# Kernel tuning notes

Hardware: AMD Instinct MI355X
Metric: run time of the kernel (lower is better)

Reference implementation:

```python
import jax, jax.numpy as jnp
import numpy as np

B, S, I, H, O, L = 64, 2048, 256, 256, 256, 2


def setup_inputs() -> dict:
    key = jax.random.key(0)
    ks = jax.random.split(key, 9)
    return {
        "x": jax.random.normal(ks[0], (B, S, I), dtype=jnp.float32),
        "w_h0": jax.random.normal(ks[1], (I, H), dtype=jnp.float32) * 0.05,
        "u_h0": jax.random.normal(ks[2], (H, H), dtype=jnp.float32) * 0.05,
        "b_h0": jax.random.uniform(ks[3], (H,), dtype=jnp.float32),
        "w_h1": jax.random.normal(ks[4], (H, H), dtype=jnp.float32) * 0.05,
        "u_h1": jax.random.normal(ks[5], (H, H), dtype=jnp.float32) * 0.05,
        "b_h1": jax.random.uniform(ks[6], (H,), dtype=jnp.float32),
        "w_q": jax.random.normal(ks[7], (H, O), dtype=jnp.float32) * 0.05,
        "b_q": jnp.zeros((O,), dtype=jnp.float32),
    }


def reference(x, w_h0, u_h0, b_h0, w_h1, u_h1, b_h1, w_q, b_q):
    batch = x.shape[0]
    h0_init = jnp.zeros((batch, H), dtype=x.dtype)
    h1_init = jnp.zeros((batch, H), dtype=x.dtype)

    def step(carry, x_t):
        h0, h1 = carry  # each [B, H]
        h0n = jnp.tanh(x_t @ w_h0 + h0 @ u_h0 + b_h0)
        h1n = jnp.tanh(h0n @ w_h1 + h1 @ u_h1 + b_h1)
        y = h1n @ w_q + b_q  # [B, O]
        return (h0n, h1n), y

    (h0_f, h1_f), ys = jax.lax.scan(step, (h0_init, h1_init),
                                    jnp.swapaxes(x, 0, 1))  # xs: [S, B, I]
    out = jnp.swapaxes(ys, 0, 1)  # [B, S, O]
    h_final = jnp.stack([h0_f, h1_f], axis=1)  # [B, L, H]
    return out, h_final
```

## Files before the change

### kernel.cpp

```cpp
#include <hip/hip_runtime.h>

#define S_LEN 2048
#define NB    64
#define HD    256

typedef _Float16 half2_t  __attribute__((ext_vector_type(2)));
typedef _Float16 half8_t  __attribute__((ext_vector_type(8)));
typedef float    floatx4  __attribute__((ext_vector_type(4)));
typedef float    floatx8  __attribute__((ext_vector_type(8)));
typedef float    floatx16 __attribute__((ext_vector_type(16)));

__device__ __forceinline__ float fdot2(half2_t a, half2_t b, float c){
#if __has_builtin(__builtin_amdgcn_fdot2)
  return __builtin_amdgcn_fdot2(a, b, c, false);
#else
  return c + (float)a[0]*(float)b[0] + (float)a[1]*(float)b[1];
#endif
}

__device__ __forceinline__ float tanh_fast(float x){
  float e = __expf(2.0f * x);
  return 1.0f - 2.0f / (e + 1.0f);
}

#define MATVEC(HS, WREG, ACC)                                                     \
  {                                                                               \
    float a0_=0.f, a1_=0.f, a2_=0.f, a3_=0.f;                                     \
    _Pragma("unroll")                                                             \
    for (int i_ = 0; i_ < 32; ++i_){                                              \
      half8_t c_ = (HS)[i_];                                                      \
      a0_ = fdot2(__builtin_shufflevector(c_, c_, 0, 1), (WREG)[4*i_+0], a0_);    \
      a1_ = fdot2(__builtin_shufflevector(c_, c_, 2, 3), (WREG)[4*i_+1], a1_);    \
      a2_ = fdot2(__builtin_shufflevector(c_, c_, 4, 5), (WREG)[4*i_+2], a2_);    \
      a3_ = fdot2(__builtin_shufflevector(c_, c_, 6, 7), (WREG)[4*i_+3], a3_);    \
    }                                                                             \
    ACC = (a0_ + a1_) + (a2_ + a3_);                                              \
  }

__launch_bounds__(768)
__global__ void rnn_kernel(const _Float16* __restrict__ A0,
                           const float* __restrict__ u_h0,
                           const float* __restrict__ w_h1,
                           const float* __restrict__ u_h1,
                           const float* __restrict__ b_h1,
                           _Float16* __restrict__ H1,
                           float* __restrict__ hfinal)
{
  const int b    = blockIdx.x;
  const int tid  = threadIdx.x;
  const int wave = tid >> 6;
  const int lane = tid & 63;
  const int group = wave >> 2;
  const int col   = ((wave & 3) << 6) | lane;

  __shared__ __align__(16) _Float16 h0buf[2][HD];
  __shared__ __align__(16) _Float16 h1buf[2][HD];
  __shared__ __align__(16) float    wpart[2][HD];

  if (tid < HD){
    h0buf[0][tid] = (_Float16)0.f; h0buf[1][tid] = (_Float16)0.f;
    h1buf[0][tid] = (_Float16)0.f; h1buf[1][tid] = (_Float16)0.f;
    wpart[0][tid] = 0.f;           wpart[1][tid] = 0.f;
  }

  const float* Wm = (group == 0) ? u_h0 : (group == 1) ? u_h1 : w_h1;
  half2_t w[128];
  #pragma unroll
  for (int i = 0; i < 128; ++i){
    float w0 = Wm[(2*i)     * HD + col];
    float w1 = Wm[(2*i + 1) * HD + col];
    half2_t p; p[0] = (_Float16)w0; p[1] = (_Float16)w1;
    w[i] = p;
  }

  const size_t base = (size_t)b * S_LEN * HD;
  const float bias = (group == 1) ? b_h1[col] : 0.f;

  _Float16 a0p0 = (_Float16)0.f, a0p1 = (_Float16)0.f;
  if (group == 0){
    a0p0 = A0[base + 0 * HD + col];
    a0p1 = A0[base + 1 * HD + col];
  }

  __syncthreads();

  for (int tau = 0; tau < S_LEN + 2; ++tau){
    if (group == 0){
      if (tau < S_LEN){
        const half8_t* hs = (const half8_t*)(&h0buf[(tau + 1) & 1][0]);
        float acc; MATVEC(hs, w, acc);
        float h = tanh_fast(acc + (float)a0p0);
        h0buf[tau & 1][col] = (_Float16)h;
        if (tau == S_LEN - 1) hfinal[(b << 9) + col] = h;
        a0p0 = a0p1;
        if (tau + 2 < S_LEN) a0p1 = A0[base + (size_t)(tau + 2) * HD + col];
      }
    } else if (group == 2){
      const int t1 = tau - 1;
      if (t1 >= 0 && t1 < S_LEN){
        const half8_t* hs = (const half8_t*)(&h0buf[t1 & 1][0]);
        float acc; MATVEC(hs, w, acc);
        wpart[t1 & 1][col] = acc;
      }
    } else {
      const int t = tau - 2;
      if (t >= 0){
        const half8_t* hs = (const half8_t*)(&h1buf[(t + 1) & 1][0]);
        float acc; MATVEC(hs, w, acc);
        float h = tanh_fast(acc + wpart[t & 1][col] + bias);
        h1buf[t & 1][col] = (_Float16)h;
        H1[base + (size_t)t * HD + col] = (_Float16)h;
        if (t == S_LEN - 1) hfinal[(b << 9) + HD + col] = h;
      }
    }
    __syncthreads();
  }
}

__global__ void prep_kernel(const float* __restrict__ w0, const float* __restrict__ wq,
                            _Float16* __restrict__ B0, _Float16* __restrict__ Bq)
{
  int i = blockIdx.x * 256 + threadIdx.x;
  for (int idx = i; idx < 65536; idx += 64 * 256){
    int k = idx >> 8, n = idx & 255;
    int sw = (k >> 3) * 2048 + n * 8 + (k & 7);
    B0[sw] = (_Float16)w0[idx];
    Bq[sw] = (_Float16)wq[idx];
  }
}

template<bool A_FP32, bool C_FP16>
__launch_bounds__(512)
__global__ void gemm256(const void* __restrict__ Ap,
                        const _Float16* __restrict__ Bsw,
                        const float* __restrict__ bias,
                        void* __restrict__ Cp)
{
  const int wave = threadIdx.x >> 6;
  const int lane = threadIdx.x & 63;
  const int r  = lane & 31;
  const int hf = lane >> 5;
  const size_t rowt = (size_t)blockIdx.x * 256 + (size_t)wave * 32;

  floatx16 acc[8];
  #pragma unroll
  for (int i = 0; i < 8; ++i)
    #pragma unroll
    for (int j = 0; j < 16; ++j) acc[i][j] = 0.f;

  const size_t arow = rowt + (size_t)r;
  #pragma unroll
  for (int ks = 0; ks < 16; ++ks){
    half8_t af;
    if (A_FP32){
      const float* A = (const float*)Ap;
      const floatx4* p = (const floatx4*)(A + arow * 256 + ks * 16 + hf * 8);
      floatx4 v0 = p[0], v1 = p[1];
      floatx8 v = __builtin_shufflevector(v0, v1, 0, 1, 2, 3, 4, 5, 6, 7);
      af = __builtin_convertvector(v, half8_t);
    } else {
      const _Float16* A = (const _Float16*)Ap;
      af = *(const half8_t*)(A + arow * 256 + ks * 16 + hf * 8);
    }
    #pragma unroll
    for (int ct = 0; ct < 8; ++ct){
      half8_t bf = *(const half8_t*)(Bsw + (size_t)(ks * 2 + hf) * 2048 + (ct * 32 + r) * 8);
      acc[ct] = __builtin_amdgcn_mfma_f32_32x32x16_f16(af, bf, acc[ct], 0, 0, 0);
    }
  }

  #pragma unroll
  for (int ct = 0; ct < 8; ++ct){
    const int col = ct * 32 + r;
    const float bc = bias[col];
    #pragma unroll
    for (int reg = 0; reg < 16; ++reg){
      const int rl = (reg & 3) + 8 * (reg >> 2) + 4 * hf;
      const size_t idx = (rowt + rl) * 256 + col;
      float v = acc[ct][reg] + bc;
      if (C_FP16) ((_Float16*)Cp)[idx] = (_Float16)v;
      else        ((float*)Cp)[idx]    = v;
    }
  }
}

extern "C" void kernel_launch(void* const* d_in, const int* in_sizes, int n_in,
                              void* d_out, int out_size, void* d_ws, size_t ws_size,
                              hipStream_t stream)
{
  (void)in_sizes; (void)n_in; (void)out_size;

  const float* x    = (const float*)d_in[0];
  const float* w_h0 = (const float*)d_in[1];
  const float* u_h0 = (const float*)d_in[2];
  const float* b_h0 = (const float*)d_in[3];
  const float* w_h1 = (const float*)d_in[4];
  const float* u_h1 = (const float*)d_in[5];
  const float* b_h1 = (const float*)d_in[6];
  const float* w_q  = (const float*)d_in[7];
  const float* b_q  = (const float*)d_in[8];

  const size_t MSH = (size_t)NB * S_LEN * HD;
  float* y    = (float*)d_out;
  float* hfin = y + MSH;

  _Float16* H1 = (_Float16*)d_ws;
  _Float16 *A0, *B0sw, *Bqsw;
  if (ws_size >= (MSH * 2 + 2 * 65536) * sizeof(_Float16)){
    A0   = H1 + MSH;
    B0sw = A0 + MSH;
    Bqsw = B0sw + 65536;
  } else {
    A0   = (_Float16*)d_out;
    B0sw = H1 + MSH;
    Bqsw = B0sw + 65536;
  }

  prep_kernel<<<dim3(64), dim3(256), 0, stream>>>(w_h0, w_q, B0sw, Bqsw);
  gemm256<true, true><<<dim3(512), dim3(512), 0, stream>>>((const void*)x, B0sw, b_h0, (void*)A0);
  rnn_kernel<<<dim3(NB), dim3(768), 0, stream>>>(A0, u_h0, w_h1, u_h1, b_h1, H1, hfin);
  gemm256<false, false><<<dim3(512), dim3(512), 0, stream>>>((const void*)H1, Bqsw, b_q, (void*)y);
}
```

Before: 2.665 ms.

## Split RNN layers into separate pipelined blocks synchronized via global flags

Replaces the single per-batch block, which ran all three matvec stages per timestep behind a block barrier, with three blocks per batch, one per stage. The blocks communicate through global ring buffers and acquire/release progress counters. This lets the layer-0 recurrence, the layer-1 input projection and the layer-1 recurrence run concurrently on different CUs. In exchange, each step adds cross-CU global-memory handoff latency and spin-waiting, and correctness depends on all blocks being co-resident.

```diff
diff --git a/kernel.cpp b/kernel.cpp
--- a/kernel.cpp
+++ b/kernel.cpp
@@ -1,8 +1,11 @@
 #include <hip/hip_runtime.h>
+#include <stdint.h>
 
 #define S_LEN 2048
 #define NB    64
 #define HD    256
+#define RING  1024
+#define RMASK 1023
 
 typedef _Float16 half2_t  __attribute__((ext_vector_type(2)));
 typedef _Float16 half8_t  __attribute__((ext_vector_type(8)));
@@ -37,33 +40,31 @@
     ACC = (a0_ + a1_) + (a2_ + a3_);                                              \
   }
 
-__launch_bounds__(768)
-__global__ void rnn_kernel(const _Float16* __restrict__ A0,
-                           const float* __restrict__ u_h0,
-                           const float* __restrict__ w_h1,
-                           const float* __restrict__ u_h1,
-                           const float* __restrict__ b_h1,
-                           _Float16* __restrict__ H1,
-                           float* __restrict__ hfinal)
-{
-  const int b    = blockIdx.x;
-  const int tid  = threadIdx.x;
-  const int wave = tid >> 6;
-  const int lane = tid & 63;
-  const int group = wave >> 2;
-  const int col   = ((wave & 3) << 6) | lane;
-
-  __shared__ __align__(16) _Float16 h0buf[2][HD];
-  __shared__ __align__(16) _Float16 h1buf[2][HD];
-  __shared__ __align__(16) float    wpart[2][HD];
-
-  if (tid < HD){
-    h0buf[0][tid] = (_Float16)0.f; h0buf[1][tid] = (_Float16)0.f;
-    h1buf[0][tid] = (_Float16)0.f; h1buf[1][tid] = (_Float16)0.f;
-    wpart[0][tid] = 0.f;           wpart[1][tid] = 0.f;
-  }
-
-  const float* Wm = (group == 0) ? u_h0 : (group == 1) ? u_h1 : w_h1;
+__launch_bounds__(256, 1)
+__global__ void rnn_pipe(const _Float16* __restrict__ A0,
+                         const float* __restrict__ u_h0,
+                         const float* __restrict__ w_h1,
+                         const float* __restrict__ u_h1,
+                         const float* __restrict__ b_h1,
+                         _Float16* __restrict__ H1,
+                         float* __restrict__ hfinal,
+                         _Float16* __restrict__ h0ring,
+                         _Float16* __restrict__ wpring,
+                         uint32_t* __restrict__ flags)
+{
+  const int stage = blockIdx.x >> 6;
+  const int b     = blockIdx.x & 63;
+  const int col   = threadIdx.x;
+
+  __shared__ __align__(16) _Float16 hbuf[2][HD];
+  hbuf[0][col] = (_Float16)0.f;
+  hbuf[1][col] = (_Float16)0.f;
+
+  uint32_t* prog0 = flags +        (b << 4);
+  uint32_t* prog2 = flags + 1024 + (b << 4);
+  uint32_t* prog1 = flags + 2048 + (b << 4);
+
+  const float* Wm = (stage == 0) ? u_h0 : (stage == 1) ? w_h1 : u_h1;
   half2_t w[128];
   #pragma unroll
   for (int i = 0; i < 128; ++i){
@@ -74,46 +75,68 @@
   }
 
   const size_t base = (size_t)b * S_LEN * HD;
-  const float bias = (group == 1) ? b_h1[col] : 0.f;
-
-  _Float16 a0p0 = (_Float16)0.f, a0p1 = (_Float16)0.f;
-  if (group == 0){
-    a0p0 = A0[base + 0 * HD + col];
-    a0p1 = A0[base + 1 * HD + col];
-  }
+  int budget = 1 << 24;
 
   __syncthreads();
 
-  for (int tau = 0; tau < S_LEN + 2; ++tau){
-    if (group == 0){
-      if (tau < S_LEN){
-        const half8_t* hs = (const half8_t*)(&h0buf[(tau + 1) & 1][0]);
-        float acc; MATVEC(hs, w, acc);
-        float h = tanh_fast(acc + (float)a0p0);
-        h0buf[tau & 1][col] = (_Float16)h;
-        if (tau == S_LEN - 1) hfinal[(b << 9) + col] = h;
-        a0p0 = a0p1;
-        if (tau + 2 < S_LEN) a0p1 = A0[base + (size_t)(tau + 2) * HD + col];
+  if (stage == 0){
+    uint32_t c2 = 0;
+    _Float16 a0n1 = A0[base + col];
+    _Float16 a0n2 = A0[base + HD + col];
+    for (int t = 0; t < S_LEN; ++t){
+      _Float16 a0c = a0n1; a0n1 = a0n2;
+      if (t + 2 < S_LEN) a0n2 = A0[base + (size_t)(t + 2) * HD + col];
+      if (t >= RING){
+        uint32_t want = (uint32_t)(t - RING + 1);
+        while (c2 < want && budget-- > 0)
+          c2 = __hip_atomic_load(prog2, __ATOMIC_ACQUIRE, __HIP_MEMORY_SCOPE_AGENT);
       }
-    } else if (group == 2){
-      const int t1 = tau - 1;
-      if (t1 >= 0 && t1 < S_LEN){
-        const half8_t* hs = (const half8_t*)(&h0buf[t1 & 1][0]);
-        float acc; MATVEC(hs, w, acc);
-        wpart[t1 & 1][col] = acc;
+      const half8_t* hs = (const half8_t*)&hbuf[(t + 1) & 1][0];
+      float acc; MATVEC(hs, w, acc);
+      float h = tanh_fast(acc + (float)a0c);
+      hbuf[t & 1][col] = (_Float16)h;
+      h0ring[(size_t)((b << 10) | (t & RMASK)) * HD + col] = (_Float16)h;
+      if (t == S_LEN - 1) hfinal[(b << 9) + col] = h;
+      __syncthreads();
+      if (col == 0)
+        __hip_atomic_store(prog0, (uint32_t)(t + 1), __ATOMIC_RELEASE, __HIP_MEMORY_SCOPE_AGENT);
+    }
+  } else if (stage == 1){
+    uint32_t c0 = 0, c1 = 0;
+    for (int t = 0; t < S_LEN; ++t){
+      if (t >= RING){
+        uint32_t want = (uint32_t)(t - RING + 1);
+        while (c1 < want && budget-- > 0)
+          c1 = __hip_atomic_load(prog1, __ATOMIC_ACQUIRE, __HIP_MEMORY_SCOPE_AGENT);
       }
-    } else {
-      const int t = tau - 2;
-      if (t >= 0){
-        const half8_t* hs = (const half8_t*)(&h1buf[(t + 1) & 1][0]);
-        float acc; MATVEC(hs, w, acc);
-        float h = tanh_fast(acc + wpart[t & 1][col] + bias);
-        h1buf[t & 1][col] = (_Float16)h;
-        H1[base + (size_t)t * HD + col] = (_Float16)h;
-        if (t == S_LEN - 1) hfinal[(b << 9) + HD + col] = h;
-      }
-    }
-    __syncthreads();
+      uint32_t want = (uint32_t)(t + 1);
+      while (c0 < want && budget-- > 0)
+        c0 = __hip_atomic_load(prog0, __ATOMIC_ACQUIRE, __HIP_MEMORY_SCOPE_AGENT);
+      const half8_t* hs = (const half8_t*)(h0ring + (size_t)((b << 10) | (t & RMASK)) * HD);
+      float acc; MATVEC(hs, w, acc);
+      wpring[(size_t)((b << 10) | (t & RMASK)) * HD + col] = (_Float16)acc;
+      __syncthreads();
+      if (col == 0)
+        __hip_atomic_store(prog2, (uint32_t)(t + 1), __ATOMIC_RELEASE, __HIP_MEMORY_SCOPE_AGENT);
+    }
+  } else {
+    const float bias = b_h1[col];
+    uint32_t c2 = 0;
+    for (int t = 0; t < S_LEN; ++t){
+      uint32_t want = (uint32_t)(t + 1);
+      while (c2 < want && budget-- > 0)
+        c2 = __hip_atomic_load(prog2, __ATOMIC_ACQUIRE, __HIP_MEMORY_SCOPE_AGENT);
+      float wp = (float)wpring[(size_t)((b << 10) | (t & RMASK)) * HD + col];
+      const half8_t* hs = (const half8_t*)&hbuf[(t + 1) & 1][0];
+      float acc; MATVEC(hs, w, acc);
+      float h = tanh_fast(acc + wp + bias);
+      hbuf[t & 1][col] = (_Float16)h;
+      H1[base + (size_t)t * HD + col] = (_Float16)h;
+      if (t == S_LEN - 1) hfinal[(b << 9) + HD + col] = h;
+      __syncthreads();
+      if (col == 0 && (((t & 15) == 15) || t == S_LEN - 1))
+        __hip_atomic_store(prog1, (uint32_t)(t + 1), __ATOMIC_RELEASE, __HIP_MEMORY_SCOPE_AGENT);
+    }
   }
 }
 
@@ -188,7 +211,7 @@
                               void* d_out, int out_size, void* d_ws, size_t ws_size,
                               hipStream_t stream)
 {
-  (void)in_sizes; (void)n_in; (void)out_size;
+  (void)in_sizes; (void)n_in; (void)out_size; (void)ws_size;
 
   const float* x    = (const float*)d_in[0];
   const float* w_h0 = (const float*)d_in[1];
@@ -201,23 +224,22 @@
   const float* b_q  = (const float*)d_in[8];
 
   const size_t MSH = (size_t)NB * S_LEN * HD;
-  float* y    = (float*)d_out;
-  float* hfin = y + MSH;
-
-  _Float16* H1 = (_Float16*)d_ws;
-  _Float16 *A0, *B0sw, *Bqsw;
-  if (ws_size >= (MSH * 2 + 2 * 65536) * sizeof(_Float16)){
-    A0   = H1 + MSH;
-    B0sw = A0 + MSH;
-    Bqsw = B0sw + 65536;
-  } else {
-    A0   = (_Float16*)d_out;
-    B0sw = H1 + MSH;
-    Bqsw = B0sw + 65536;
-  }
-
+
+  float*    y      = (float*)d_out;
+  float*    hfin   = y + MSH;
+  _Float16* A0     = (_Float16*)d_out;
+  _Float16* h0ring = A0 + MSH;
+  _Float16* wpring = h0ring + MSH / 2;
+
+  _Float16* H1    = (_Float16*)d_ws;
+  _Float16* B0sw  = H1 + MSH;
+  _Float16* Bqsw  = B0sw + 65536;
+  uint32_t* flags = (uint32_t*)(Bqsw + 65536);
+
+  hipMemsetAsync((void*)flags, 0, 3072 * sizeof(uint32_t), stream);
   prep_kernel<<<dim3(64), dim3(256), 0, stream>>>(w_h0, w_q, B0sw, Bqsw);
   gemm256<true, true><<<dim3(512), dim3(512), 0, stream>>>((const void*)x, B0sw, b_h0, (void*)A0);
-  rnn_kernel<<<dim3(NB), dim3(768), 0, stream>>>(A0, u_h0, w_h1, u_h1, b_h1, H1, hfin);
+  rnn_pipe<<<dim3(192), dim3(256), 0, stream>>>(A0, u_h0, w_h1, u_h1, b_h1,
+                                                H1, hfin, h0ring, wpring, flags);
   gemm256<false, false><<<dim3(512), dim3(512), 0, stream>>>((const void*)H1, Bqsw, b_q, (void*)y);
 }
```

New measurement: 7.291 ms. 2.74x slower.
